# Optimization experiments

Measured on AMD Instinct MI355X. Metric: run time of the kernel, lower is better.

## Reference

```python
import jax, jax.numpy as jnp
import numpy as np

N_NODES = 2000
GCN_OUT = 8
HID = 256
N_STEPS_OUT = 4


def setup_inputs() -> dict:
    key = jax.random.key(0)
    ks = jax.random.split(key, 16)
    B, S, N, E, F, H = 32, 24, N_NODES, 16000, GCN_OUT, HID
    I = F * N  # LSTM input size = gcn_out_features * num_nodes
    s = 0.05
    inp = {
        "x_sequences": jax.random.normal(ks[0], (B, S, N), jnp.float32),
        "edge_index": jax.random.randint(ks[1], (B, S, 2, E), 0, N, jnp.int32),
        "edge_distances": jax.random.uniform(ks[2], (B, S, E), jnp.float32),
        # CustomGCNLayer params (linear 1->F)
        "W_gcn": jax.random.normal(ks[3], (1, F), jnp.float32) * s,
        "b_gcn": jnp.zeros((F,), jnp.float32),
        # 2-layer LSTM (PyTorch layout: [4H, in], gate order i,f,g,o)
        "Wih0": jax.random.normal(ks[4], (4 * H, I), jnp.float32) * s,
        "Whh0": jax.random.normal(ks[5], (4 * H, H), jnp.float32) * s,
        "bih0": jnp.zeros((4 * H,), jnp.float32),
        "bhh0": jnp.zeros((4 * H,), jnp.float32),
        "Wih1": jax.random.normal(ks[6], (4 * H, H), jnp.float32) * s,
        "Whh1": jax.random.normal(ks[7], (4 * H, H), jnp.float32) * s,
        "bih1": jnp.zeros((4 * H,), jnp.float32),
        "bhh1": jnp.zeros((4 * H,), jnp.float32),
        # fc: hidden -> n_steps_out * num_nodes * num_node_features
        "fc_W": jax.random.normal(ks[8], (N_STEPS_OUT * N, H), jnp.float32) * s,
        "fc_b": jnp.zeros((N_STEPS_OUT * N,), jnp.float32),
    }
    return inp


def _lstm_layer(x, Wih, Whh, bih, bhh):
    # x: [B, S, in] -> hs: [B, S, H]
    B = x.shape[0]
    H = Whh.shape[1]
    b = bih + bhh

    def step(carry, xt):
        h, c = carry
        gates = xt @ Wih.T + h @ Whh.T + b  # [B, 4H]
        i, f, g, o = jnp.split(gates, 4, axis=-1)
        i = jax.nn.sigmoid(i)
        f = jax.nn.sigmoid(f)
        g = jnp.tanh(g)
        o = jax.nn.sigmoid(o)
        c = f * c + i * g
        h = o * jnp.tanh(c)
        return (h, c), h

    init = (jnp.zeros((B, H), x.dtype), jnp.zeros((B, H), x.dtype))
    _, hs = jax.lax.scan(step, init, x.transpose(1, 0, 2))  # time-major
    return hs.transpose(1, 0, 2)


def reference(x_sequences, edge_index, edge_distances, W_gcn, b_gcn,
              Wih0, Whh0, bih0, bhh0, Wih1, Whh1, bih1, bhh1, fc_W, fc_b):
    B, S, N = x_sequences.shape
    F = W_gcn.shape[1]
    # GCN layer (batched over all B*S graph snapshots):
    # h = x @ W + b ; out[i] = sum_{(j->i)} dist_e * h[j]
    h = x_sequences[..., None] * W_gcn[0] + b_gcn        # [B,S,N,F]
    src = edge_index[:, :, 0].reshape(B * S, -1)         # [BS,E]
    dst = edge_index[:, :, 1].reshape(B * S, -1)
    dist = edge_distances.reshape(B * S, -1)
    h2 = h.reshape(B * S, N, F)
    msgs = jnp.take_along_axis(h2, src[:, :, None], axis=1) * dist[..., None]  # [BS,E,F]
    agg = jax.vmap(lambda m, d: jax.ops.segment_sum(m, d, num_segments=N))(msgs, dst)
    gcn_seq = jnp.tanh(agg.reshape(B, S, N * F))         # [B,S,N*F]

    h1 = _lstm_layer(gcn_seq, Wih0, Whh0, bih0, bhh0)
    h2l = _lstm_layer(h1, Wih1, Whh1, bih1, bhh1)
    last = jnp.tanh(h2l)[:, -1, :]                       # [B,H]
    out = last @ fc_W.T + fc_b                           # [B, n_steps_out*N]
    n_steps_out = fc_b.shape[0] // N
    return out.reshape(B, n_steps_out, N)                # num_node_features=1 squeezed
```

## Files before the change

### kernel.cpp

```cpp
#include <hip/hip_runtime.h>

#define DEVINL __device__ __forceinline__

typedef __attribute__((ext_vector_type(8))) short bf16x8;
typedef __attribute__((ext_vector_type(4))) float f32x4;
typedef _Float16 half2_t __attribute__((ext_vector_type(2)));
typedef _Float16 f16x8 __attribute__((ext_vector_type(8)));

DEVINL unsigned short f2bf(float f) {
  unsigned int u = __float_as_uint(f);
  u += 0x7FFFu + ((u >> 16) & 1u);
  return (unsigned short)(u >> 16);
}
DEVINL unsigned short f2h(float f) {
  return __builtin_bit_cast(unsigned short, (_Float16)f);
}
DEVINL float sigmf(float x) { return 1.f / (1.f + __expf(-x)); }
DEVINL float tanh_fast(float x) { float e = __expf(2.f * x); return 1.f - 2.f / (e + 1.f); }

DEVINL float fdot2u(unsigned int h, unsigned int w, float acc) {
  return __builtin_amdgcn_fdot2(__builtin_bit_cast(half2_t, h),
                                __builtin_bit_cast(half2_t, w), acc, false);
}


__global__ __launch_bounds__(256) void conv_bf16(const float* __restrict__ in,
                                                 unsigned short* __restrict__ out) {
  int id = blockIdx.x * 256 + threadIdx.x;
  float4 v = *(const float4*)&in[(size_t)id * 4];
  unsigned int a = (unsigned int)f2bf(v.x) | ((unsigned int)f2bf(v.y) << 16);
  unsigned int b = (unsigned int)f2bf(v.z) | ((unsigned int)f2bf(v.w) << 16);
  *(uint2*)&out[(size_t)id * 4] = make_uint2(a, b);
}

__global__ __launch_bounds__(256) void conv_f16(const float* __restrict__ in,
                                                unsigned short* __restrict__ out) {
  int id = blockIdx.x * 256 + threadIdx.x;
  out[id] = f2h(in[id]);
}

__global__ __launch_bounds__(256) void pack_whh_g(const float* __restrict__ in,
                                                  uint2* __restrict__ out) {
  int id = blockIdx.x * 256 + threadIdx.x;
  int g = id >> 14;
  int rem = id & 16383;
  int u2 = rem >> 8;
  int c = rem & 255;
  int col = (c >> 6) * 256 + g * 64 + (c & 63);
  float4 v = *(const float4*)&in[col * 256 + u2 * 4];
  unsigned int p0 = (unsigned int)f2h(v.x) | ((unsigned int)f2h(v.y) << 16);
  unsigned int p1 = (unsigned int)f2h(v.z) | ((unsigned int)f2h(v.w) << 16);
  out[id] = make_uint2(p0, p1);
}

#define FXSCALE 1048576.f
#define FXINV   (1.f / 1048576.f)

__global__ __launch_bounds__(1024) void gcn_kernel(
    const float* __restrict__ x, const int* __restrict__ ei, const float* __restrict__ ed,
    const float* __restrict__ Wg, const float* __restrict__ bg,
    unsigned short* __restrict__ G) {
  __shared__ float xs[2000];
  __shared__ int Ai[2000];
  __shared__ int Di[2000];
  int bs = blockIdx.x;
  int tid = threadIdx.x;
  for (int i = tid; i < 2000; i += 1024) {
    xs[i] = x[(size_t)bs * 2000 + i];
    Ai[i] = 0; Di[i] = 0;
  }
  __syncthreads();
  const int* srcp = ei + (size_t)bs * 32000;
  const int* dstp = srcp + 16000;
  const float* dp = ed + (size_t)bs * 16000;
  for (int i = tid; i < 4000; i += 1024) {
    int4 s4 = ((const int4*)srcp)[i];
    int4 d4 = ((const int4*)dstp)[i];
    float4 w4 = ((const float4*)dp)[i];
    atomicAdd(&Ai[d4.x], __float2int_rn(w4.x * xs[s4.x] * FXSCALE));
    atomicAdd(&Di[d4.x], __float2int_rn(w4.x * FXSCALE));
    atomicAdd(&Ai[d4.y], __float2int_rn(w4.y * xs[s4.y] * FXSCALE));
    atomicAdd(&Di[d4.y], __float2int_rn(w4.y * FXSCALE));
    atomicAdd(&Ai[d4.z], __float2int_rn(w4.z * xs[s4.z] * FXSCALE));
    atomicAdd(&Di[d4.z], __float2int_rn(w4.z * FXSCALE));
    atomicAdd(&Ai[d4.w], __float2int_rn(w4.w * xs[s4.w] * FXSCALE));
    atomicAdd(&Di[d4.w], __float2int_rn(w4.w * FXSCALE));
  }
  __syncthreads();
  float wreg[8], breg[8];
#pragma unroll
  for (int f = 0; f < 8; ++f) { wreg[f] = Wg[f]; breg[f] = bg[f]; }
  for (int n = tid; n < 2000; n += 1024) {
    float a  = (float)Ai[n] * FXINV;
    float dd = (float)Di[n] * FXINV;
    unsigned int u[4];
#pragma unroll
    for (int p = 0; p < 4; ++p) {
      float v0 = tanh_fast(wreg[2 * p] * a + breg[2 * p] * dd);
      float v1 = tanh_fast(wreg[2 * p + 1] * a + breg[2 * p + 1] * dd);
      u[p] = (unsigned int)f2bf(v0) | ((unsigned int)f2bf(v1) << 16);
    }
    *(uint4*)&G[(size_t)bs * 16000 + n * 8] = make_uint4(u[0], u[1], u[2], u[3]);
  }
}

__global__ __launch_bounds__(256) void gemm_bt(
    const unsigned short* __restrict__ A, const unsigned short* __restrict__ B,
    float* __restrict__ Cp) {
  __shared__ __align__(16) unsigned short As[128 * 32];
  __shared__ __align__(16) unsigned short Bs[128 * 32];
  const int K = 16000;
  int nt = blockIdx.x;
  int mt = blockIdx.y;
  int ks = blockIdx.z;
  int m0 = mt * 128, n0 = nt * 128;
  int tid = threadIdx.x;
  int lane = tid & 63;
  int w = tid >> 6;
  int wm = (w >> 1) * 64, wn = (w & 1) * 64;
  int fr = lane & 15;
  int kg = lane >> 4;

  f32x4 acc[4][4] = {};
  const unsigned short* Ag = A + (size_t)m0 * K + ks * 1600;
  const unsigned short* Bg = B + (size_t)n0 * K + ks * 1600;

  for (int kk = 0; kk < 1600; kk += 32) {
#pragma unroll
    for (int q = 0; q < 2; ++q) {
      int c = q * 256 + tid;
      int row = c >> 2;
      int ko = (c & 3) * 8;
      *(uint4*)&As[c * 8] = *(const uint4*)&Ag[(size_t)row * K + kk + ko];
      *(uint4*)&Bs[c * 8] = *(const uint4*)&Bg[(size_t)row * K + kk + ko];
    }
    __syncthreads();
    bf16x8 aF[4], bF[4];
#pragma unroll
    for (int i = 0; i < 4; ++i)
      aF[i] = *(const bf16x8*)&As[(wm + i * 16 + fr) * 32 + kg * 8];
#pragma unroll
    for (int i = 0; i < 4; ++i)
      bF[i] = *(const bf16x8*)&Bs[(wn + i * 16 + fr) * 32 + kg * 8];
#pragma unroll
    for (int i = 0; i < 4; ++i)
#pragma unroll
      for (int j = 0; j < 4; ++j)
        acc[i][j] = __builtin_amdgcn_mfma_f32_16x16x32_bf16(aF[i], bF[j], acc[i][j], 0, 0, 0);
    __syncthreads();
  }
  float* Co = Cp + (size_t)ks * 768 * 1024;
  int mr = (lane >> 4) * 4;
#pragma unroll
  for (int i = 0; i < 4; ++i)
#pragma unroll
    for (int j = 0; j < 4; ++j) {
      int n = n0 + wn + j * 16 + fr;
#pragma unroll
      for (int r = 0; r < 4; ++r) {
        int m = m0 + wm + i * 16 + mr + r;
        Co[(size_t)m * 1024 + n] = acc[i][j][r];
      }
    }
}

__global__ __launch_bounds__(256) void reduce_z0(
    const float* __restrict__ Cp, const float* __restrict__ bih,
    const float* __restrict__ bhh, float* __restrict__ Z0) {
  int id = blockIdx.x * 256 + threadIdx.x;
  float s = bih[id & 1023] + bhh[id & 1023];
#pragma unroll
  for (int p = 0; p < 10; ++p) s += Cp[(size_t)p * 786432 + id];
  Z0[id] = s;
}

__global__ __launch_bounds__(1024) void lstm_sync2(
    const float* __restrict__ Z, const uint2* __restrict__ WPG,
    unsigned int* __restrict__ Hex, unsigned short* __restrict__ Hout,
    float* __restrict__ lastOut, int tagBase) {
  __shared__ __align__(16) uint2 Wl2[64 * 256];
  __shared__ float gparts[1024];
  __shared__ __align__(8) unsigned short h16[256];
  int bid = blockIdx.x;
  int b = bid >> 2, g = bid & 3;
  int tid = threadIdx.x;
  int lane = tid & 63;
  int c = tid & 255;
  int kh = __builtin_amdgcn_readfirstlane(tid >> 8);
  int q = c >> 6, r = c & 63;
  int col = q * 256 + g * 64 + r;

  const uint2* wsrc = WPG + (size_t)g * 16384;
  for (int i = tid; i < 16384; i += 1024) Wl2[i] = wsrc[i];
  if (tid < 128) ((unsigned int*)h16)[tid] = 0;
  __syncthreads();

  float cst = 0.f;
  const size_t b24 = (size_t)b * 24;

#pragma unroll 1
  for (int t = 0; t < 24; ++t) {
    uint2 hv = *(const uint2*)&((const unsigned int*)h16)[lane * 2];
    float acc = (kh == 0) ? Z[(b24 + t) * 1024 + col] : 0.f;
#pragma unroll
    for (int j = 0; j < 16; ++j) {
      const int u2i = kh * 16 + j;
      uint2 w2 = Wl2[u2i * 256 + c];
      unsigned int h0 = (unsigned int)__builtin_amdgcn_readlane((int)hv.x, u2i);
      unsigned int h1 = (unsigned int)__builtin_amdgcn_readlane((int)hv.y, u2i);
      acc = fdot2u(h0, w2.x, acc);
      acc = fdot2u(h1, w2.y, acc);
    }
    gparts[tid] = acc;
    __syncthreads();
    unsigned int* HexS = Hex + (t & 1) * 8192 + b * 256;
    if (tid < 64) {
      float i_ = gparts[tid]       + gparts[tid + 256]  + gparts[tid + 512]  + gparts[tid + 768];
      float f_ = gparts[tid + 64]  + gparts[tid + 320]  + gparts[tid + 576]  + gparts[tid + 832];
      float g_ = gparts[tid + 128] + gparts[tid + 384]  + gparts[tid + 640]  + gparts[tid + 896];
      float o_ = gparts[tid + 192] + gparts[tid + 448]  + gparts[tid + 704]  + gparts[tid + 960];
      float ig = sigmf(i_), fg = sigmf(f_);
      float gg = tanh_fast(g_), og = sigmf(o_);
      cst = fg * cst + ig * gg;
      float h = og * tanh_fast(cst);
      unsigned short hh = f2h(h);
      h16[g * 64 + tid] = hh;
      __hip_atomic_store(&HexS[g * 64 + tid],
                         (unsigned int)hh | ((unsigned int)(tagBase + t + 1) << 16),
                         __ATOMIC_RELAXED, __HIP_MEMORY_SCOPE_AGENT);
      if (Hout) Hout[(b24 + t) * 256 + g * 64 + tid] = hh;
      if (lastOut && t == 23) lastOut[b * 256 + g * 64 + tid] = tanh_fast(h);
    }
    if (t == 23) break;
    if (tid < 256 && (tid >> 6) != g) {
      const unsigned int tag = (unsigned int)(tagBase + t + 1);
      unsigned int v;
      do {
        v = __hip_atomic_load(&HexS[tid], __ATOMIC_RELAXED, __HIP_MEMORY_SCOPE_AGENT);
      } while ((v >> 16) != tag);
      h16[tid] = (unsigned short)(v & 0xFFFFu);
    }
    __syncthreads();
  }
}

__global__ __launch_bounds__(256) void gemm_z1_mfma(
    const unsigned short* __restrict__ A, const unsigned short* __restrict__ B,
    const float* __restrict__ bih, const float* __restrict__ bhh,
    float* __restrict__ Z1) {
  __shared__ __align__(16) unsigned short As[128 * 32];
  __shared__ __align__(16) unsigned short Bs[128 * 32];
  const int K = 256;
  int nt = blockIdx.x;
  int mt = blockIdx.y;
  int m0 = mt * 128, n0 = nt * 128;
  int tid = threadIdx.x;
  int lane = tid & 63;
  int w = tid >> 6;
  int wm = (w >> 1) * 64, wn = (w & 1) * 64;
  int fr = lane & 15;
  int kg = lane >> 4;

  f32x4 acc[4][4] = {};
  const unsigned short* Ag = A + (size_t)m0 * K;
  const unsigned short* Bg = B + (size_t)n0 * K;

  for (int kk = 0; kk < 256; kk += 32) {
#pragma unroll
    for (int q = 0; q < 2; ++q) {
      int c = q * 256 + tid;
      int row = c >> 2;
      int ko = (c & 3) * 8;
      *(uint4*)&As[c * 8] = *(const uint4*)&Ag[(size_t)row * K + kk + ko];
      *(uint4*)&Bs[c * 8] = *(const uint4*)&Bg[(size_t)row * K + kk + ko];
    }
    __syncthreads();
    f16x8 aF[4], bF[4];
#pragma unroll
    for (int i = 0; i < 4; ++i)
      aF[i] = *(const f16x8*)&As[(wm + i * 16 + fr) * 32 + kg * 8];
#pragma unroll
    for (int i = 0; i < 4; ++i)
      bF[i] = *(const f16x8*)&Bs[(wn + i * 16 + fr) * 32 + kg * 8];
#pragma unroll
    for (int i = 0; i < 4; ++i)
#pragma unroll
      for (int j = 0; j < 4; ++j)
        acc[i][j] = __builtin_amdgcn_mfma_f32_16x16x32_f16(aF[i], bF[j], acc[i][j], 0, 0, 0);
    __syncthreads();
  }
  int mr = (lane >> 4) * 4;
#pragma unroll
  for (int j = 0; j < 4; ++j) {
    int n = n0 + wn + j * 16 + fr;
    float bias = bih[n] + bhh[n];
#pragma unroll
    for (int i = 0; i < 4; ++i) {
#pragma unroll
      for (int r = 0; r < 4; ++r) {
        int m = m0 + wm + i * 16 + mr + r;
        Z1[(size_t)m * 1024 + n] = acc[i][j][r] + bias;
      }
    }
  }
}

__global__ __launch_bounds__(256) void fc_kernel(
    const float* __restrict__ last, const float* __restrict__ fcW,
    const float* __restrict__ fcb, float* __restrict__ out) {
  __shared__ float ls[8][256];
  int tid = threadIdx.x;
  int o = blockIdx.x * 256 + tid;
  int b0 = blockIdx.y * 8;
  for (int i = tid; i < 2048; i += 256)
    ls[i >> 8][i & 255] = last[(b0 + (i >> 8)) * 256 + (i & 255)];
  __syncthreads();
  if (o < 8000) {
    float acc[8] = {};
    for (int k = 0; k < 256; k += 4) {
      float4 wv = *(const float4*)&fcW[(size_t)o * 256 + k];
#pragma unroll
      for (int b = 0; b < 8; ++b)
        acc[b] += wv.x * ls[b][k] + wv.y * ls[b][k + 1] + wv.z * ls[b][k + 2] + wv.w * ls[b][k + 3];
    }
    float bias = fcb[o];
#pragma unroll
    for (int b = 0; b < 8; ++b) out[(size_t)(b0 + b) * 8000 + o] = acc[b] + bias;
  }
}

extern "C" void kernel_launch(void* const* d_in, const int* in_sizes, int n_in,
                              void* d_out, int out_size, void* d_ws, size_t ws_size,
                              hipStream_t stream) {
  const float* x    = (const float*)d_in[0];
  const int*   ei   = (const int*)d_in[1];
  const float* ed   = (const float*)d_in[2];
  const float* Wg   = (const float*)d_in[3];
  const float* bg   = (const float*)d_in[4];
  const float* Wih0 = (const float*)d_in[5];
  const float* Whh0 = (const float*)d_in[6];
  const float* bih0 = (const float*)d_in[7];
  const float* bhh0 = (const float*)d_in[8];
  const float* Wih1 = (const float*)d_in[9];
  const float* Whh1 = (const float*)d_in[10];
  const float* bih1 = (const float*)d_in[11];
  const float* bhh1 = (const float*)d_in[12];
  const float* fcW  = (const float*)d_in[13];
  const float* fcb  = (const float*)d_in[14];
  float* out = (float*)d_out;

  char* ws = (char*)d_ws;
  unsigned short* Gbf  = (unsigned short*)(ws);
  unsigned short* W0bf = (unsigned short*)(ws + 24576000);
  float* Zpart = (float*)(ws + 57344000);
  float* Z0    = (float*)(ws + 88801280);
  uint2* WPG0  = (uint2*)(ws + 91947008);
  uint2* WPG1  = (uint2*)(ws + 92471296);
  unsigned short* W1h = (unsigned short*)(ws + 92995584);
  unsigned short* H1  = (unsigned short*)(ws + 94044160);
  float* Z1    = (float*)(ws + 94830592);
  float* lastb = (float*)(ws + 97976320);
  unsigned int* Hex0 = (unsigned int*)(ws + 98009088);
  unsigned int* Hex1 = (unsigned int*)(ws + 98074624);

  hipMemsetAsync(Hex0, 0, 131072, stream);
  conv_bf16<<<16000, 256, 0, stream>>>(Wih0, W0bf);
  pack_whh_g<<<256, 256, 0, stream>>>(Whh0, WPG0);
  pack_whh_g<<<256, 256, 0, stream>>>(Whh1, WPG1);
  conv_f16<<<1024, 256, 0, stream>>>(Wih1, (unsigned short*)W1h);
  gcn_kernel<<<768, 1024, 0, stream>>>(x, ei, ed, Wg, bg, Gbf);
  gemm_bt<<<dim3(8, 6, 10), 256, 0, stream>>>(Gbf, W0bf, Zpart);
  reduce_z0<<<3072, 256, 0, stream>>>(Zpart, bih0, bhh0, Z0);
  lstm_sync2<<<128, 1024, 0, stream>>>(Z0, WPG0, Hex0, H1, nullptr, 0);
  gemm_z1_mfma<<<dim3(8, 6), 256, 0, stream>>>(H1, W1h, bih1, bhh1, Z1);
  lstm_sync2<<<128, 1024, 0, stream>>>(Z1, WPG1, Hex1, nullptr, lastb, 100);
  fc_kernel<<<dim3(32, 4), 256, 0, stream>>>(lastb, fcW, fcb, out);
}
```

Measured before the change: 257.0 us.

## Double-buffer GEMM with direct global-to-LDS loads and skip degree atomics for zero bias

The big bf16 GEMM now loads tiles straight from global memory into LDS with global_load_lds and double-buffers them, so the next tile's load overlaps the current tile's MFMAs. The second GEMM also uses the direct-to-LDS loads. The GCN kernel batches its edge loads two at a time and skips the degree atomics when all GCN biases are zero. The bias check is a runtime test on the inputs, not a hardcoded assumption. There is a risk that the wait for the async LDS loads before the barrier is not enforced.

```diff
diff --git a/kernel.cpp b/kernel.cpp
--- a/kernel.cpp
+++ b/kernel.cpp
@@ -21,6 +21,12 @@
 DEVINL float fdot2u(unsigned int h, unsigned int w, float acc) {
   return __builtin_amdgcn_fdot2(__builtin_bit_cast(half2_t, h),
                                 __builtin_bit_cast(half2_t, w), acc, false);
+}
+
+DEVINL void gload_lds16(const void* g, void* l) {
+  __builtin_amdgcn_global_load_lds(
+      (const __attribute__((address_space(1))) void*)g,
+      (__attribute__((address_space(3))) void*)l, 16, 0, 0);
 }
 
 
@@ -69,22 +75,42 @@
     xs[i] = x[(size_t)bs * 2000 + i];
     Ai[i] = 0; Di[i] = 0;
   }
+  bool bgz = (bg[0] == 0.f) && (bg[1] == 0.f) && (bg[2] == 0.f) && (bg[3] == 0.f) &&
+             (bg[4] == 0.f) && (bg[5] == 0.f) && (bg[6] == 0.f) && (bg[7] == 0.f);
   __syncthreads();
-  const int* srcp = ei + (size_t)bs * 32000;
-  const int* dstp = srcp + 16000;
-  const float* dp = ed + (size_t)bs * 16000;
-  for (int i = tid; i < 4000; i += 1024) {
-    int4 s4 = ((const int4*)srcp)[i];
-    int4 d4 = ((const int4*)dstp)[i];
-    float4 w4 = ((const float4*)dp)[i];
-    atomicAdd(&Ai[d4.x], __float2int_rn(w4.x * xs[s4.x] * FXSCALE));
-    atomicAdd(&Di[d4.x], __float2int_rn(w4.x * FXSCALE));
-    atomicAdd(&Ai[d4.y], __float2int_rn(w4.y * xs[s4.y] * FXSCALE));
-    atomicAdd(&Di[d4.y], __float2int_rn(w4.y * FXSCALE));
-    atomicAdd(&Ai[d4.z], __float2int_rn(w4.z * xs[s4.z] * FXSCALE));
-    atomicAdd(&Di[d4.z], __float2int_rn(w4.z * FXSCALE));
-    atomicAdd(&Ai[d4.w], __float2int_rn(w4.w * xs[s4.w] * FXSCALE));
-    atomicAdd(&Di[d4.w], __float2int_rn(w4.w * FXSCALE));
+  const int4* srcp = (const int4*)(ei + (size_t)bs * 32000);
+  const int4* dstp = (const int4*)(ei + (size_t)bs * 32000 + 16000);
+  const float4* dp = (const float4*)(ed + (size_t)bs * 16000);
+
+#pragma unroll
+  for (int half = 0; half < 2; ++half) {
+    int ia = tid + half * 2048;
+    int ib = ia + 1024;
+    bool okb = (ib < 4000);
+    int ibc = okb ? ib : 0;
+    int4 sA = srcp[ia], dA = dstp[ia];
+    float4 wA = dp[ia];
+    int4 sB = srcp[ibc], dB = dstp[ibc];
+    float4 wB = dp[ibc];
+    if (!okb) wB = make_float4(0.f, 0.f, 0.f, 0.f);
+    atomicAdd(&Ai[dA.x], __float2int_rn(wA.x * xs[sA.x] * FXSCALE));
+    atomicAdd(&Ai[dA.y], __float2int_rn(wA.y * xs[sA.y] * FXSCALE));
+    atomicAdd(&Ai[dA.z], __float2int_rn(wA.z * xs[sA.z] * FXSCALE));
+    atomicAdd(&Ai[dA.w], __float2int_rn(wA.w * xs[sA.w] * FXSCALE));
+    atomicAdd(&Ai[dB.x], __float2int_rn(wB.x * xs[sB.x] * FXSCALE));
+    atomicAdd(&Ai[dB.y], __float2int_rn(wB.y * xs[sB.y] * FXSCALE));
+    atomicAdd(&Ai[dB.z], __float2int_rn(wB.z * xs[sB.z] * FXSCALE));
+    atomicAdd(&Ai[dB.w], __float2int_rn(wB.w * xs[sB.w] * FXSCALE));
+    if (!bgz) {
+      atomicAdd(&Di[dA.x], __float2int_rn(wA.x * FXSCALE));
+      atomicAdd(&Di[dA.y], __float2int_rn(wA.y * FXSCALE));
+      atomicAdd(&Di[dA.z], __float2int_rn(wA.z * FXSCALE));
+      atomicAdd(&Di[dA.w], __float2int_rn(wA.w * FXSCALE));
+      atomicAdd(&Di[dB.x], __float2int_rn(wB.x * FXSCALE));
+      atomicAdd(&Di[dB.y], __float2int_rn(wB.y * FXSCALE));
+      atomicAdd(&Di[dB.z], __float2int_rn(wB.z * FXSCALE));
+      atomicAdd(&Di[dB.w], __float2int_rn(wB.w * FXSCALE));
+    }
   }
   __syncthreads();
   float wreg[8], breg[8];
@@ -107,8 +133,8 @@
 __global__ __launch_bounds__(256) void gemm_bt(
     const unsigned short* __restrict__ A, const unsigned short* __restrict__ B,
     float* __restrict__ Cp) {
-  __shared__ __align__(16) unsigned short As[128 * 32];
-  __shared__ __align__(16) unsigned short Bs[128 * 32];
+  __shared__ __align__(16) unsigned short As[2][128 * 32];
+  __shared__ __align__(16) unsigned short Bs[2][128 * 32];
   const int K = 16000;
   int nt = blockIdx.x;
   int mt = blockIdx.y;
@@ -125,23 +151,30 @@
   const unsigned short* Ag = A + (size_t)m0 * K + ks * 1600;
   const unsigned short* Bg = B + (size_t)n0 * K + ks * 1600;
 
-  for (int kk = 0; kk < 1600; kk += 32) {
-#pragma unroll
-    for (int q = 0; q < 2; ++q) {
-      int c = q * 256 + tid;
-      int row = c >> 2;
-      int ko = (c & 3) * 8;
-      *(uint4*)&As[c * 8] = *(const uint4*)&Ag[(size_t)row * K + kk + ko];
-      *(uint4*)&Bs[c * 8] = *(const uint4*)&Bg[(size_t)row * K + kk + ko];
-    }
-    __syncthreads();
+  int row0 = tid >> 2,            ko0 = (tid & 3) * 8,        cb0 = (tid & ~63);
+  int row1 = (256 + tid) >> 2,    ko1 = (tid & 3) * 8,        cb1 = 256 + (tid & ~63);
+
+#define STAGE_BT(buf, kk)                                                     \
+  do {                                                                        \
+    gload_lds16(&Ag[(size_t)row0 * K + (kk) + ko0], &As[buf][cb0 * 8]);       \
+    gload_lds16(&Bg[(size_t)row0 * K + (kk) + ko0], &Bs[buf][cb0 * 8]);       \
+    gload_lds16(&Ag[(size_t)row1 * K + (kk) + ko1], &As[buf][cb1 * 8]);       \
+    gload_lds16(&Bg[(size_t)row1 * K + (kk) + ko1], &Bs[buf][cb1 * 8]);       \
+  } while (0)
+
+  STAGE_BT(0, 0);
+  __syncthreads();
+#pragma unroll 1
+  for (int it = 0; it < 50; ++it) {
+    int cur = it & 1;
+    if (it < 49) STAGE_BT(cur ^ 1, (it + 1) * 32);
     bf16x8 aF[4], bF[4];
 #pragma unroll
     for (int i = 0; i < 4; ++i)
-      aF[i] = *(const bf16x8*)&As[(wm + i * 16 + fr) * 32 + kg * 8];
-#pragma unroll
-    for (int i = 0; i < 4; ++i)
-      bF[i] = *(const bf16x8*)&Bs[(wn + i * 16 + fr) * 32 + kg * 8];
+      aF[i] = *(const bf16x8*)&As[cur][(wm + i * 16 + fr) * 32 + kg * 8];
+#pragma unroll
+    for (int i = 0; i < 4; ++i)
+      bF[i] = *(const bf16x8*)&Bs[cur][(wn + i * 16 + fr) * 32 + kg * 8];
 #pragma unroll
     for (int i = 0; i < 4; ++i)
 #pragma unroll
@@ -149,6 +182,7 @@
         acc[i][j] = __builtin_amdgcn_mfma_f32_16x16x32_bf16(aF[i], bF[j], acc[i][j], 0, 0, 0);
     __syncthreads();
   }
+#undef STAGE_BT
   float* Co = Cp + (size_t)ks * 768 * 1024;
   int mr = (lane >> 4) * 4;
 #pragma unroll
@@ -271,8 +305,9 @@
       int c = q * 256 + tid;
       int row = c >> 2;
       int ko = (c & 3) * 8;
-      *(uint4*)&As[c * 8] = *(const uint4*)&Ag[(size_t)row * K + kk + ko];
-      *(uint4*)&Bs[c * 8] = *(const uint4*)&Bg[(size_t)row * K + kk + ko];
+      int cb = q * 256 + (tid & ~63);
+      gload_lds16(&Ag[(size_t)row * K + kk + ko], &As[cb * 8]);
+      gload_lds16(&Bg[(size_t)row * K + kk + ko], &Bs[cb * 8]);
     }
     __syncthreads();
     f16x8 aF[4], bF[4];
```

Result: faster. 250.7 us (-2.5%).
